# Kernel tuning notes

Measured on AMD Instinct MI355X. Metric: run time of the kernel, lower is better.

The kernel has to match this reference:

```python
import jax, jax.numpy as jnp
import numpy as np

C_S, C_Z, C_H = 384, 128, 32
EPS = 1e-5


def setup_inputs() -> dict:
    key = jax.random.key(0)
    ks = jax.random.split(key, 8)
    N, L = 1, 512
    s = jax.random.normal(ks[0], (N, L, C_S), dtype=jnp.float32)
    ln_gamma = jnp.ones((C_S,), jnp.float32)
    ln_beta = jnp.zeros((C_S,), jnp.float32)
    sc = 1.0 / np.sqrt(C_S)
    w1 = jax.random.normal(ks[1], (C_S, C_H), jnp.float32) * sc
    b1 = jax.random.normal(ks[2], (C_H,), jnp.float32) * 0.02
    w2 = jax.random.normal(ks[3], (C_S, C_H), jnp.float32) * sc
    b2 = jax.random.normal(ks[4], (C_H,), jnp.float32) * 0.02
    w_out = jax.random.normal(ks[5], (C_H * C_H, C_Z), jnp.float32) * (1.0 / C_H)
    b_out = jax.random.normal(ks[6], (C_Z,), jnp.float32) * 0.02
    return {"s": s, "ln_gamma": ln_gamma, "ln_beta": ln_beta,
            "w1": w1, "b1": b1, "w2": w2, "b2": b2,
            "w_out": w_out, "b_out": b_out}


def reference(s, ln_gamma, ln_beta, w1, b1, w2, b2, w_out, b_out):
    # LayerNorm over c_s
    mu = jnp.mean(s, axis=-1, keepdims=True)
    var = jnp.mean(jnp.square(s - mu), axis=-1, keepdims=True)
    sn = (s - mu) * jax.lax.rsqrt(var + EPS) * ln_gamma + ln_beta
    # two projections: [N, L, c_hidden]
    a = jnp.einsum('nlc,ch->nlh', sn, w1) + b1
    b = jnp.einsum('nlc,ch->nlh', sn, w2) + b2
    # outer product + linear_out fused: (a_i ⊗ b_j) contracted with W_out
    w3 = w_out.reshape(C_H, C_H, C_Z)  # [h_a, h_b, c_z]
    z = jnp.einsum('nia,njb,abz->nijz', a, b, w3) + b_out
    return z  # [N, L, L, c_z]
```

## Files before the change

### kernel.cpp

```cpp
#include <hip/hip_runtime.h>

#define CS 384
#define CH 32
#define CZ 128
#define LL 512
#define C4 (CZ * CH)
#define EPSV 1e-5f

typedef __attribute__((ext_vector_type(8))) short bf16x8;
typedef __attribute__((ext_vector_type(4))) float f32x4;

static __device__ __forceinline__ unsigned short f2bf(float x) {
  union { float f; unsigned int u; } c; c.f = x;
  unsigned int r = c.u + 0x7FFFu + ((c.u >> 16) & 1u);
  return (unsigned short)(r >> 16);
}
static __device__ __forceinline__ unsigned int pk2(float lo, float hi) {
  return (unsigned int)f2bf(lo) | ((unsigned int)f2bf(hi) << 16);
}

__global__ __launch_bounds__(256) void prep_kernel(
    const float* __restrict__ s, const float* __restrict__ gamma,
    const float* __restrict__ beta,
    const float* __restrict__ w1, const float* __restrict__ b1,
    const float* __restrict__ w2, const float* __restrict__ b2,
    const float* __restrict__ w_out,
    unsigned short* __restrict__ Abf, unsigned short* __restrict__ Bbf,
    unsigned short* __restrict__ Wt) {
  __shared__ union {
    struct { float sn[CS]; float red[256]; float wred[8]; } ln;
    float wl[CH * CZ];
  } sm;
  int tid = threadIdx.x;

  if (blockIdx.x < LL) {
    int l = blockIdx.x;
    const float* srow = s + l * CS;
    float lsum = 0.f, lsq = 0.f;
    for (int c = tid; c < CS; c += 256) {
      float x = srow[c]; sm.ln.sn[c] = x; lsum += x; lsq += x * x;
    }
    #pragma unroll
    for (int off = 32; off > 0; off >>= 1) {
      lsum += __shfl_down(lsum, off);
      lsq  += __shfl_down(lsq, off);
    }
    int wv = tid >> 6;
    if ((tid & 63) == 0) { sm.ln.wred[wv] = lsum; sm.ln.wred[4 + wv] = lsq; }
    __syncthreads();
    float s1 = sm.ln.wred[0] + sm.ln.wred[1] + sm.ln.wred[2] + sm.ln.wred[3];
    float s2 = sm.ln.wred[4] + sm.ln.wred[5] + sm.ln.wred[6] + sm.ln.wred[7];
    float mu = s1 * (1.0f / CS);
    float var = s2 * (1.0f / CS) - mu * mu;
    float rstd = rsqrtf(var + EPSV);

    for (int c = tid; c < CS; c += 256)
      sm.ln.sn[c] = (sm.ln.sn[c] - mu) * rstd * gamma[c] + beta[c];
    __syncthreads();

    int o = tid & 63, q = tid >> 6;
    int h = o & 31;
    const float* w = (o < CH) ? w1 : w2;
    float acc = 0.f;
    int c0 = q * 96;
    #pragma unroll 8
    for (int c = c0; c < c0 + 96; ++c) acc += sm.ln.sn[c] * w[c * CH + h];
    sm.ln.red[tid] = acc; __syncthreads();
    if (tid < 64) {
      float r = sm.ln.red[tid] + sm.ln.red[tid + 64] + sm.ln.red[tid + 128] +
                sm.ln.red[tid + 192];
      if (o < CH) Abf[l * CH + h] = f2bf(r + b1[h]);
      else        Bbf[l * CH + h] = f2bf(r + b2[h]);
    }
  } else {
    int a = blockIdx.x - LL;
    const float4* Wg = (const float4*)(w_out + (size_t)a * CH * CZ);
    float4* Wl4 = (float4*)sm.wl;
    #pragma unroll
    for (int v = 0; v < 4; ++v) Wl4[tid + v * 256] = Wg[tid + v * 256];
    __syncthreads();
    int z = tid >> 1, bh = tid & 1;
    unsigned int dw[8];
    #pragma unroll
    for (int k = 0; k < 8; ++k) {
      unsigned short lo = f2bf(sm.wl[(bh * 16 + 2 * k) * CZ + z]);
      unsigned short hi = f2bf(sm.wl[(bh * 16 + 2 * k + 1) * CZ + z]);
      dw[k] = (unsigned int)lo | ((unsigned int)hi << 16);
    }
    unsigned int* dst =
        (unsigned int*)((char*)Wt + ((size_t)z * CH + a) * 64 + bh * 32);
    *(uint4*)dst = make_uint4(dw[0], dw[1], dw[2], dw[3]);
    *(uint4*)(dst + 4) = make_uint4(dw[4], dw[5], dw[6], dw[7]);
  }
}

__global__ __launch_bounds__(64) void tmat_kernel(
    const unsigned short* __restrict__ Bbf, const unsigned short* __restrict__ Wt,
    unsigned short* __restrict__ Tt) {
  int jt = blockIdx.x;
  int cq = blockIdx.y;
  int l = threadIdx.x;
  int q = l >> 4, r = l & 15;
  bf16x8 bfrag = *(const bf16x8*)(Bbf + (size_t)(jt * 16 + r) * CH + 8 * q);
  int j = jt * 16 + r;
  f32x4 zer = {0.f, 0.f, 0.f, 0.f};
  #pragma unroll
  for (int t = 0; t < 8; ++t) {
    int cbase = cq * 128 + t * 16;
    bf16x8 wfrag = *(const bf16x8*)(Wt + (size_t)(cbase + r) * CH + 8 * q);
    f32x4 acc = __builtin_amdgcn_mfma_f32_16x16x32_bf16(wfrag, bfrag, zer, 0, 0, 0);
    uint2 st;
    st.x = pk2(acc[0], acc[1]);
    st.y = pk2(acc[2], acc[3]);
    *(uint2*)(&Tt[(size_t)j * C4 + cbase + 4 * q]) = st;
  }
}

__global__ __launch_bounds__(256) void outer_mfma(
    const unsigned short* __restrict__ Abf, const unsigned short* __restrict__ Tt,
    const float* __restrict__ b_out, float* __restrict__ out) {
  unsigned n = blockIdx.x;
  unsigned xcd = n & 7, idx = n >> 3;
  unsigned wu = xcd * 256 + idx;
  int it = wu >> 9;
  int j  = wu & 511;
  int tid = threadIdx.x;
  int w = tid >> 6, l = tid & 63, q = l >> 4, r = l & 15;
  int ib = it * 128 + w * 32;

  bf16x8 af0 = *(const bf16x8*)(Abf + (size_t)(ib + r) * CH + 8 * q);
  bf16x8 af1 = *(const bf16x8*)(Abf + (size_t)(ib + 16 + r) * CH + 8 * q);
  const unsigned short* Tj = Tt + (size_t)j * C4;

  #pragma unroll
  for (int zt = 0; zt < 8; ++zt) {
    f32x4 bo = *(const f32x4*)(b_out + zt * 16 + 4 * q);
    bf16x8 tf = *(const bf16x8*)(Tj + (size_t)(zt * 16 + r) * CH + 8 * q);
    f32x4 a0 = __builtin_amdgcn_mfma_f32_16x16x32_bf16(tf, af0, bo, 0, 0, 0);
    f32x4 a1 = __builtin_amdgcn_mfma_f32_16x16x32_bf16(tf, af1, bo, 0, 0, 0);
    float* o0 = out + ((size_t)(ib + r) * LL + j) * CZ + zt * 16 + 4 * q;
    float* o1 = out + ((size_t)(ib + 16 + r) * LL + j) * CZ + zt * 16 + 4 * q;
    *(f32x4*)o0 = a0;
    *(f32x4*)o1 = a1;
  }
}

extern "C" void kernel_launch(void* const* d_in, const int* in_sizes, int n_in,
                              void* d_out, int out_size, void* d_ws, size_t ws_size,
                              hipStream_t stream) {
  const float* s     = (const float*)d_in[0];
  const float* gam   = (const float*)d_in[1];
  const float* bet   = (const float*)d_in[2];
  const float* w1    = (const float*)d_in[3];
  const float* b1    = (const float*)d_in[4];
  const float* w2    = (const float*)d_in[5];
  const float* b2    = (const float*)d_in[6];
  const float* w_out = (const float*)d_in[7];
  const float* b_out = (const float*)d_in[8];
  float* out = (float*)d_out;

  char* ws = (char*)d_ws;
  unsigned short* Abf = (unsigned short*)(ws);
  unsigned short* Bbf = (unsigned short*)(ws + 32768);
  unsigned short* Wt  = (unsigned short*)(ws + 65536);
  unsigned short* Tt  = (unsigned short*)(ws + 327680);

  prep_kernel<<<LL + CH, 256, 0, stream>>>(s, gam, bet, w1, b1, w2, b2, w_out,
                                           Abf, Bbf, Wt);
  tmat_kernel<<<dim3(32, 32), 64, 0, stream>>>(Bbf, Wt, Tt);
  outer_mfma<<<2048, 256, 0, stream>>>(Abf, Tt, b_out, out);
}
```

Measured before the change: 44.77 us.

## Retile outer product kernel so each block covers 16 rows by 64 columns

The final outer-product kernel is reorganized. Each block of 512 threads now handles 16 output rows (i) and 64 columns (j), with each wave looping over 8 j values. Before, each block handled 128 rows for a single j with an XCD-aware swizzle. The bias fragments are hoisted out of the loop and the A fragment is loaded once per wave. The goal is a fully contiguous 64-column output span per i row, for better write coalescing and DRAM locality. In exchange the grid shrinks to 256 blocks and the XCD swizzle is removed, which may leave CUs underfilled and reduce Tt reuse across rows.

Result: faster. 42.31 us (-5.5%).

```diff
diff --git a/kernel.cpp b/kernel.cpp
--- a/kernel.cpp
+++ b/kernel.cpp
@@ -116,32 +116,36 @@
   }
 }
 
-__global__ __launch_bounds__(256) void outer_mfma(
+__global__ __launch_bounds__(512) void outer_mfma(
     const unsigned short* __restrict__ Abf, const unsigned short* __restrict__ Tt,
     const float* __restrict__ b_out, float* __restrict__ out) {
   unsigned n = blockIdx.x;
-  unsigned xcd = n & 7, idx = n >> 3;
-  unsigned wu = xcd * 256 + idx;
-  int it = wu >> 9;
-  int j  = wu & 511;
+  int jt = n & 7;
+  int it = n >> 3;
   int tid = threadIdx.x;
   int w = tid >> 6, l = tid & 63, q = l >> 4, r = l & 15;
-  int ib = it * 128 + w * 32;
+  int ib = it * 16;
 
-  bf16x8 af0 = *(const bf16x8*)(Abf + (size_t)(ib + r) * CH + 8 * q);
-  bf16x8 af1 = *(const bf16x8*)(Abf + (size_t)(ib + 16 + r) * CH + 8 * q);
-  const unsigned short* Tj = Tt + (size_t)j * C4;
+  bf16x8 af = *(const bf16x8*)(Abf + (size_t)(ib + r) * CH + 8 * q);
 
+  f32x4 bo[8];
   #pragma unroll
-  for (int zt = 0; zt < 8; ++zt) {
-    f32x4 bo = *(const f32x4*)(b_out + zt * 16 + 4 * q);
-    bf16x8 tf = *(const bf16x8*)(Tj + (size_t)(zt * 16 + r) * CH + 8 * q);
-    f32x4 a0 = __builtin_amdgcn_mfma_f32_16x16x32_bf16(tf, af0, bo, 0, 0, 0);
-    f32x4 a1 = __builtin_amdgcn_mfma_f32_16x16x32_bf16(tf, af1, bo, 0, 0, 0);
-    float* o0 = out + ((size_t)(ib + r) * LL + j) * CZ + zt * 16 + 4 * q;
-    float* o1 = out + ((size_t)(ib + 16 + r) * LL + j) * CZ + zt * 16 + 4 * q;
-    *(f32x4*)o0 = a0;
-    *(f32x4*)o1 = a1;
+  for (int zt = 0; zt < 8; ++zt) bo[zt] = *(const f32x4*)(b_out + zt * 16 + 4 * q);
+
+  int j0 = jt * 64 + w * 8;
+  float* orow = out + ((size_t)(ib + r) * LL) * CZ;
+
+  #pragma unroll 2
+  for (int jj = 0; jj < 8; ++jj) {
+    int j = j0 + jj;
+    const unsigned short* Tj = Tt + (size_t)j * C4;
+    float* oj = orow + (size_t)j * CZ;
+    #pragma unroll
+    for (int zt = 0; zt < 8; ++zt) {
+      bf16x8 tf = *(const bf16x8*)(Tj + (size_t)(zt * 16 + r) * CH + 8 * q);
+      f32x4 d = __builtin_amdgcn_mfma_f32_16x16x32_bf16(tf, af, bo[zt], 0, 0, 0);
+      *(f32x4*)(oj + zt * 16 + 4 * q) = d;
+    }
   }
 }
 
@@ -168,5 +172,5 @@
   prep_kernel<<<LL + CH, 256, 0, stream>>>(s, gam, bet, w1, b1, w2, b2, w_out,
                                            Abf, Bbf, Wt);
   tmat_kernel<<<dim3(32, 32), 64, 0, stream>>>(Bbf, Wt, Tt);
-  outer_mfma<<<2048, 256, 0, stream>>>(Abf, Tt, b_out, out);
+  outer_mfma<<<256, 512, 0, stream>>>(Abf, Tt, b_out, out);
 }
```
